# Performance work log

Measured on AMD Instinct MI355X. Metric: run time of the kernel, lower is better.

The kernel has to match this reference:

```python
import jax, jax.numpy as jnp
import numpy as np

HEADS = 8
DIM = 512
DIM_HEAD = 64          # dim // 8
LANDMARKS = 256        # dim // 2
PINV_ITERS = 6
KERNEL = 33            # residual depthwise conv kernel
EPS_LN = 1e-5


def setup_inputs() -> dict:
    key = jax.random.key(0)
    ks = jax.random.split(key, 4)
    b, n = 4, 4096
    x = jax.random.normal(ks[0], (b, n, DIM), dtype=jnp.float32)
    ln_g = jnp.ones((DIM,), jnp.float32)
    ln_b = jnp.zeros((DIM,), jnp.float32)
    w_qkv = jax.random.normal(ks[1], (3 * HEADS * DIM_HEAD, DIM), jnp.float32) * 0.02
    w_out = jax.random.normal(ks[2], (DIM, HEADS * DIM_HEAD), jnp.float32) * 0.02
    b_out = jnp.zeros((DIM,), jnp.float32)
    res_w = jax.random.normal(ks[3], (HEADS, 1, KERNEL, 1), jnp.float32) * 0.05
    return {"x": x, "ln_g": ln_g, "ln_b": ln_b, "w_qkv": w_qkv,
            "w_out": w_out, "b_out": b_out, "res_w": res_w}


def _moore_penrose_pinv(x, iters):
    # x: [b, h, m, m]; global (whole-tensor) max of row/col abs-sums, as in torch impl
    abs_x = jnp.abs(x)
    col = abs_x.sum(-1).max()
    row = abs_x.sum(-2).max()
    z = jnp.swapaxes(x, -1, -2) / (col * row)
    I = jnp.eye(x.shape[-1], dtype=x.dtype)
    for _ in range(iters):
        xz = x @ z
        z = 0.25 * z @ (13.0 * I - (xz @ (15.0 * I - (xz @ (7.0 * I - xz)))))
    return z


def reference(x, ln_g, ln_b, w_qkv, w_out, b_out, res_w):
    b, n, d = x.shape
    # pre-norm LayerNorm
    mu = x.mean(-1, keepdims=True)
    var = ((x - mu) ** 2).mean(-1, keepdims=True)
    xn = (x - mu) * jax.lax.rsqrt(var + EPS_LN) * ln_g + ln_b

    qkv = xn @ w_qkv.T                                  # [b, n, 3*h*dh]
    q, k, v = jnp.split(qkv, 3, axis=-1)
    to_heads = lambda t: t.reshape(b, n, HEADS, DIM_HEAD).transpose(0, 2, 1, 3)
    q = to_heads(q) * (DIM_HEAD ** -0.5)                # [b, h, n, dh]
    k = to_heads(k)
    v = to_heads(v)

    m = LANDMARKS
    l = n // m                                          # n chosen multiple of m (no pad)
    q_l = q.reshape(b, HEADS, m, l, DIM_HEAD).mean(3)   # [b, h, m, dh]
    k_l = k.reshape(b, HEADS, m, l, DIM_HEAD).mean(3)

    attn1 = jax.nn.softmax(jnp.einsum('bhid,bhjd->bhij', q, k_l), -1)    # [b,h,n,m]
    attn2 = jax.nn.softmax(jnp.einsum('bhid,bhjd->bhij', q_l, k_l), -1)  # [b,h,m,m]
    attn3 = jax.nn.softmax(jnp.einsum('bhid,bhjd->bhij', q_l, k), -1)    # [b,h,m,n]

    attn2_inv = _moore_penrose_pinv(attn2, PINV_ITERS)
    out = (attn1 @ attn2_inv) @ (attn3 @ v)             # [b, h, n, dh]

    # residual depthwise conv over sequence dim: v as NCHW (C=heads, H=n, W=dh)
    pad = KERNEL // 2
    res = jax.lax.conv_general_dilated(
        v, res_w, window_strides=(1, 1), padding=((pad, pad), (0, 0)),
        dimension_numbers=('NCHW', 'OIHW', 'NCHW'), feature_group_count=HEADS)
    out = out + res

    out = out.transpose(0, 2, 1, 3).reshape(b, n, HEADS * DIM_HEAD)
    out = out @ w_out.T + b_out                         # to_out Linear (dropout=eval identity)
    return x + out
```

## Files before the change

kernel.cpp:

```cpp
#include <hip/hip_runtime.h>
#include <hip/hip_bf16.h>
#include <math.h>


using bf16x8 = __attribute__((ext_vector_type(8))) short;
using f32x4  = __attribute__((ext_vector_type(4))) float;

static __device__ __forceinline__ f32x4 MFMA16(bf16x8 a, bf16x8 b, f32x4 c) {
    return __builtin_amdgcn_mfma_f32_16x16x32_bf16(a, b, c, 0, 0, 0);
}
static __device__ __forceinline__ unsigned short f2b(float f) {
    union { float f; unsigned u; } x; x.f = f;
    unsigned r = x.u + 0x7FFFu + ((x.u >> 16) & 1u);
    return (unsigned short)(r >> 16);
}
static __device__ __forceinline__ float b2f(unsigned short b) {
    union { unsigned u; float f; } x; x.u = ((unsigned)b) << 16; return x.f;
}

__global__ __launch_bounds__(256) void ln_kernel(const float* __restrict__ x,
                                                 const float* __restrict__ g,
                                                 const float* __restrict__ b,
                                                 unsigned short* __restrict__ xn) {
    int row = blockIdx.x;
    const float* xr = x + (size_t)row * 512;
    int t = threadIdx.x;
    float v0 = xr[t], v1 = xr[t + 256];
    __shared__ float red[4];
    float s = v0 + v1;
#pragma unroll
    for (int off = 32; off; off >>= 1) s += __shfl_down(s, off);
    if ((t & 63) == 0) red[t >> 6] = s;
    __syncthreads();
    float mean = (red[0] + red[1] + red[2] + red[3]) * (1.0f / 512.0f);
    __syncthreads();
    float d0 = v0 - mean, d1 = v1 - mean;
    float q2 = d0 * d0 + d1 * d1;
#pragma unroll
    for (int off = 32; off; off >>= 1) q2 += __shfl_down(q2, off);
    if ((t & 63) == 0) red[t >> 6] = q2;
    __syncthreads();
    float var = (red[0] + red[1] + red[2] + red[3]) * (1.0f / 512.0f);
    float inv = rsqrtf(var + 1e-5f);
    unsigned short* o = xn + (size_t)row * 512;
    o[t]       = f2b(d0 * inv * g[t]       + b[t]);
    o[t + 256] = f2b(d1 * inv * g[t + 256] + b[t + 256]);
}

__global__ void cvt_kernel(const float* __restrict__ wqkv, const float* __restrict__ wout,
                           unsigned short* __restrict__ wqkvb, unsigned short* __restrict__ woutb) {
    int idx = blockIdx.x * 256 + threadIdx.x;
    if (idx < 786432) wqkvb[idx] = f2b(wqkv[idx]);
    else woutb[idx - 786432] = f2b(wout[idx - 786432]);
}

template<int MODE>
__global__ __launch_bounds__(256) void gemm_mfma(const unsigned short* __restrict__ A,
                                                 const unsigned short* __restrict__ Bw,
                                                 unsigned short* __restrict__ qb,
                                                 unsigned short* __restrict__ kb,
                                                 unsigned short* __restrict__ vb,
                                                 const float* __restrict__ bias,
                                                 const float* __restrict__ xres,
                                                 float* __restrict__ out) {
    const int K = 512;
    __shared__ unsigned short As[128][40];
    __shared__ unsigned short Bs[128][40];
    int t = threadIdx.x;
    int w = t >> 6, l = t & 63, lr = l & 15, g = l >> 4;
    int wm = w >> 1, wn = w & 1;
    int row0 = blockIdx.x * 128, col0 = blockIdx.y * 128;
    f32x4 acc[4][4];
#pragma unroll
    for (int i = 0; i < 4; ++i)
#pragma unroll
        for (int j = 0; j < 4; ++j) acc[i][j] = (f32x4)0.f;
    int srow = t >> 1, sh = t & 1;
    for (int kt = 0; kt < K; kt += 32) {
        const unsigned short* as = A + (size_t)(row0 + srow) * K + kt + sh * 16;
        *(uint4*)&As[srow][sh * 16]     = *(const uint4*)as;
        *(uint4*)&As[srow][sh * 16 + 8] = *(const uint4*)(as + 8);
        const unsigned short* bs = Bw + (size_t)(col0 + srow) * K + kt + sh * 16;
        *(uint4*)&Bs[srow][sh * 16]     = *(const uint4*)bs;
        *(uint4*)&Bs[srow][sh * 16 + 8] = *(const uint4*)(bs + 8);
        __syncthreads();
        bf16x8 a[4], b[4];
#pragma unroll
        for (int mt = 0; mt < 4; ++mt) a[mt] = *(const bf16x8*)&As[wm * 64 + mt * 16 + lr][g * 8];
#pragma unroll
        for (int nt = 0; nt < 4; ++nt) b[nt] = *(const bf16x8*)&Bs[wn * 64 + nt * 16 + lr][g * 8];
#pragma unroll
        for (int mt = 0; mt < 4; ++mt)
#pragma unroll
            for (int nt = 0; nt < 4; ++nt) acc[mt][nt] = MFMA16(a[mt], b[nt], acc[mt][nt]);
        __syncthreads();
    }
#pragma unroll
    for (int mt = 0; mt < 4; ++mt) {
#pragma unroll
        for (int nt = 0; nt < 4; ++nt) {
#pragma unroll
            for (int r = 0; r < 4; ++r) {
                int row = row0 + wm * 64 + mt * 16 + g * 4 + r;
                int col = col0 + wn * 64 + nt * 16 + lr;
                float val = acc[mt][nt][r];
                if (MODE == 0) {
                    int bb = row >> 12, nn = row & 4095;
                    int which = col >> 9, rem = col & 511;
                    int hh = rem >> 6, dd = rem & 63;
                    size_t di = (((size_t)(bb * 8 + hh)) * 4096 + nn) * 64 + dd;
                    if (which == 0) qb[di] = f2b(val * 0.125f);
                    else if (which == 1) kb[di] = f2b(val);
                    else vb[di] = f2b(val);
                } else {
                    out[(size_t)row * 512 + col] = val + bias[col] + xres[(size_t)row * 512 + col];
                }
            }
        }
    }
}

__global__ __launch_bounds__(256) void vt_kernel(const unsigned short* __restrict__ vb,
                                                 unsigned short* __restrict__ vtb) {
    int n0 = blockIdx.x * 64, bh = blockIdx.y;
    __shared__ unsigned short tl[64][72];
    int t = threadIdx.x;
#pragma unroll
    for (int u = 0; u < 2; ++u) {
        int cid = t * 2 + u;
        int r = cid >> 3, c8 = (cid & 7) << 3;
        uint4 vv = *(const uint4*)(vb + ((size_t)bh * 4096 + n0 + r) * 64 + c8);
        unsigned short* pv = (unsigned short*)&vv;
#pragma unroll
        for (int i = 0; i < 8; ++i) tl[c8 + i][r] = pv[i];
    }
    __syncthreads();
#pragma unroll
    for (int u = 0; u < 2; ++u) {
        int cid = t * 2 + u;
        int r = cid >> 3, c8 = (cid & 7) << 3;
        *(uint4*)(vtb + ((size_t)bh * 64 + r) * 4096 + n0 + c8) = *(uint4*)&tl[r][c8];
    }
}

__global__ void landmark_kernel(const unsigned short* __restrict__ q,
                                const unsigned short* __restrict__ k,
                                float* __restrict__ ql, float* __restrict__ kl,
                                unsigned short* __restrict__ qlb, unsigned short* __restrict__ klb) {
    int idx = blockIdx.x * 256 + threadIdx.x;
    int dh = idx & 63, mi = (idx >> 6) & 255, bh = idx >> 14;
    size_t base = ((size_t)bh * 4096 + mi * 16) * 64 + dh;
    float sq = 0, sk = 0;
#pragma unroll
    for (int j = 0; j < 16; ++j) { sq += b2f(q[base + (size_t)j * 64]); sk += b2f(k[base + (size_t)j * 64]); }
    sq *= 0.0625f; sk *= 0.0625f;
    ql[idx] = sq; kl[idx] = sk;
    qlb[idx] = f2b(sq); klb[idx] = f2b(sk);
}

__global__ __launch_bounds__(256) void conv_kernel(const unsigned short* __restrict__ v,
                                                   const float* __restrict__ rw,
                                                   float* __restrict__ outh) {
    int idx = blockIdx.x * 256 + threadIdx.x;
    int o = idx & 7, n = (idx >> 3) & 4095, bh = idx >> 15;
    int h = bh & 7;
    const unsigned short* vb = v + (((size_t)bh) << 18) + o * 8;
    float acc[8];
#pragma unroll
    for (int i = 0; i < 8; ++i) acc[i] = 0.f;
#pragma unroll
    for (int tt = 0; tt < 33; ++tt) {
        int j = n + tt - 16;
        if (j >= 0 && j < 4096) {
            uint4 pv = *(const uint4*)(vb + (size_t)j * 64);
            const unsigned short* pp = (const unsigned short*)&pv;
            float wgt = rw[h * 33 + tt];
#pragma unroll
            for (int i = 0; i < 8; ++i) acc[i] = fmaf(wgt, b2f(pp[i]), acc[i]);
        }
    }
    float4 r0, r1;
    r0.x = acc[0]; r0.y = acc[1]; r0.z = acc[2]; r0.w = acc[3];
    r1.x = acc[4]; r1.y = acc[5]; r1.z = acc[6]; r1.w = acc[7];
    *(float4*)(outh + (size_t)idx * 8)     = r0;
    *(float4*)(outh + (size_t)idx * 8 + 4) = r1;
}

__global__ __launch_bounds__(256) void attn2_kernel(const float* __restrict__ ql,
                                                    const float* __restrict__ kl,
                                                    float* __restrict__ a2) {
    int bh = blockIdx.x >> 8, i = blockIdx.x & 255;
    int t = threadIdx.x;
    __shared__ float qrow[64];
    __shared__ float red[4];
    if (t < 64) qrow[t] = ql[((size_t)bh * 256 + i) * 64 + t];
    __syncthreads();
    const float* krow = kl + ((size_t)bh * 256 + t) * 64;
    float s = 0;
#pragma unroll
    for (int c = 0; c < 64; c += 4) {
        float4 kv = *(const float4*)(krow + c);
        s = fmaf(qrow[c], kv.x, s); s = fmaf(qrow[c + 1], kv.y, s);
        s = fmaf(qrow[c + 2], kv.z, s); s = fmaf(qrow[c + 3], kv.w, s);
    }
    float p = __expf(s);
    float sum = p;
#pragma unroll
    for (int off = 32; off; off >>= 1) sum += __shfl_down(sum, off);
    if ((t & 63) == 0) red[t >> 6] = sum;
    __syncthreads();
    float tot = red[0] + red[1] + red[2] + red[3];
    a2[((size_t)bh * 256 + i) * 256 + t] = p / tot;
}

__global__ __launch_bounds__(256) void colmax_kernel(const float* __restrict__ a2,
                                                     unsigned* __restrict__ scal) {
    int bh = blockIdx.x, t = threadIdx.x;
    const float* m = a2 + (size_t)bh * 65536;
    float cs = 0;
    for (int i = 0; i < 256; ++i) cs += m[i * 256 + t];
#pragma unroll
    for (int off = 32; off; off >>= 1) cs = fmaxf(cs, __shfl_down(cs, off));
    __shared__ float red[4];
    if ((t & 63) == 0) red[t >> 6] = cs;
    __syncthreads();
    if (t == 0) {
        float mx = fmaxf(fmaxf(red[0], red[1]), fmaxf(red[2], red[3]));
        atomicMax(scal, __float_as_uint(mx));
    }
}

__global__ __launch_bounds__(256) void z0_kernel(const float* __restrict__ a2,
                                                 const float* __restrict__ scal,
                                                 float* __restrict__ z) {
    int bh = blockIdx.z;
    int ib = blockIdx.x * 64, jb = blockIdx.y * 64;
    __shared__ float tl[64][65];
    float c = 1.0f / *scal;
    int t = threadIdx.x;
#pragma unroll
    for (int u = 0; u < 16; ++u) {
        int idx = t + 256 * u;
        int r = idx >> 6, cc = idx & 63;
        tl[r][cc] = a2[(size_t)bh * 65536 + (size_t)(jb + r) * 256 + ib + cc];
    }
    __syncthreads();
#pragma unroll
    for (int u = 0; u < 16; ++u) {
        int idx = t + 256 * u;
        int r = idx >> 6, cc = idx & 63;
        z[(size_t)bh * 65536 + (size_t)(ib + r) * 256 + jb + cc] = tl[cc][r] * c;
    }
}

__global__ __launch_bounds__(256) void bgemm_mfma_split(const float* __restrict__ A,
                                                        const float* __restrict__ B,
                                                        float* __restrict__ D,
                                                        const float* __restrict__ E,
                                                        float alpha, float gamma) {
    int s = blockIdx.z;
    A += (size_t)s * 65536; B += (size_t)s * 65536; D += (size_t)s * 65536;
    const float* Ep = E ? E + (size_t)s * 65536 : nullptr;
    __shared__ unsigned short Ah[64][40], Al[64][40], Bh[64][40], Bl[64][40];
    int t = threadIdx.x;
    int w = t >> 6, l = t & 63, lr = l & 15, g = l >> 4;
    int wm = w >> 1, wn = w & 1;
    int bm = blockIdx.x, bn = blockIdx.y;
    f32x4 acc[2][2];
#pragma unroll
    for (int i = 0; i < 2; ++i)
#pragma unroll
        for (int j = 0; j < 2; ++j) acc[i][j] = (f32x4)0.f;
    int arow = t >> 2, akq = (t & 3) * 8;
    int bkr = t >> 3, bnq = (t & 7) * 8;
    for (int kt = 0; kt < 256; kt += 32) {
        const float* ap = A + (size_t)(bm * 64 + arow) * 256 + kt + akq;
        float4 a0 = *(const float4*)ap;
        float4 a1 = *(const float4*)(ap + 4);
        float av[8] = {a0.x, a0.y, a0.z, a0.w, a1.x, a1.y, a1.z, a1.w};
#pragma unroll
        for (int i = 0; i < 8; ++i) {
            unsigned short hi = f2b(av[i]);
            Ah[arow][akq + i] = hi;
            Al[arow][akq + i] = f2b(av[i] - b2f(hi));
        }
        const float* bp = B + (size_t)(kt + bkr) * 256 + bn * 64 + bnq;
        float4 b0 = *(const float4*)bp;
        float4 b1 = *(const float4*)(bp + 4);
        float bv[8] = {b0.x, b0.y, b0.z, b0.w, b1.x, b1.y, b1.z, b1.w};
#pragma unroll
        for (int i = 0; i < 8; ++i) {
            unsigned short hi = f2b(bv[i]);
            Bh[bnq + i][bkr] = hi;
            Bl[bnq + i][bkr] = f2b(bv[i] - b2f(hi));
        }
        __syncthreads();
        bf16x8 ah[2], al_[2], bh[2], bl_[2];
#pragma unroll
        for (int mf = 0; mf < 2; ++mf) {
            ah[mf]  = *(const bf16x8*)&Ah[wm * 32 + mf * 16 + lr][g * 8];
            al_[mf] = *(const bf16x8*)&Al[wm * 32 + mf * 16 + lr][g * 8];
        }
#pragma unroll
        for (int nf = 0; nf < 2; ++nf) {
            bh[nf]  = *(const bf16x8*)&Bh[wn * 32 + nf * 16 + lr][g * 8];
            bl_[nf] = *(const bf16x8*)&Bl[wn * 32 + nf * 16 + lr][g * 8];
        }
#pragma unroll
        for (int mf = 0; mf < 2; ++mf)
#pragma unroll
            for (int nf = 0; nf < 2; ++nf) {
                acc[mf][nf] = MFMA16(ah[mf], bh[nf], acc[mf][nf]);
                acc[mf][nf] = MFMA16(ah[mf], bl_[nf], acc[mf][nf]);
                acc[mf][nf] = MFMA16(al_[mf], bh[nf], acc[mf][nf]);
            }
        __syncthreads();
    }
#pragma unroll
    for (int mf = 0; mf < 2; ++mf) {
#pragma unroll
        for (int nf = 0; nf < 2; ++nf) {
#pragma unroll
            for (int r = 0; r < 4; ++r) {
                int row = bm * 64 + wm * 32 + mf * 16 + g * 4 + r;
                int col = bn * 64 + wn * 32 + nf * 16 + lr;
                float val = alpha * acc[mf][nf][r];
                if (Ep) val = fmaf(gamma, Ep[(size_t)row * 256 + col], val);
                D[(size_t)row * 256 + col] = val;
            }
        }
    }
}

__global__ __launch_bounds__(256) void bgemm_w2t(const float* __restrict__ A,
                                                 const float* __restrict__ B,
                                                 unsigned short* __restrict__ w2t) {
    const int M = 256, N = 64, K = 256;
    int s = blockIdx.z;
    int bm = blockIdx.x;
    A += (size_t)s * M * K; B += (size_t)s * K * N;
    __shared__ float As[32][67];
    __shared__ float Bs[32][68];
    int t = threadIdx.x;
    int tm = t & 15, tn = t >> 4;
    float acc[4][4];
#pragma unroll
    for (int i = 0; i < 4; ++i)
#pragma unroll
        for (int j = 0; j < 4; ++j) acc[i][j] = 0.f;
    for (int kt = 0; kt < K; kt += 32) {
#pragma unroll
        for (int u = 0; u < 2; ++u) {
            int fid = t + 256 * u;
            int r = fid >> 3, kg = (fid & 7) << 2;
            float4 av = *(const float4*)(A + (size_t)(bm * 64 + r) * K + kt + kg);
            As[kg + 0][r] = av.x; As[kg + 1][r] = av.y; As[kg + 2][r] = av.z; As[kg + 3][r] = av.w;
            int kr = fid >> 4, cg = (fid & 15) << 2;
            if (cg < N) {
                float4 bv = *(const float4*)(B + (size_t)(kt + kr) * N + cg);
                *(float4*)(&Bs[kr][cg]) = bv;
            }
        }
        __syncthreads();
#pragma unroll
        for (int kk = 0; kk < 32; ++kk) {
            float a[4], bb[4];
#pragma unroll
            for (int i = 0; i < 4; ++i) a[i] = As[kk][tm * 4 + i];
#pragma unroll
            for (int j = 0; j < 4; ++j) bb[j] = Bs[kk][(tn & 15) * 4 + j];
#pragma unroll
            for (int i = 0; i < 4; ++i)
#pragma unroll
                for (int j = 0; j < 4; ++j) acc[i][j] = fmaf(a[i], bb[j], acc[i][j]);
        }
        __syncthreads();
    }
    if (tn < 16) {
#pragma unroll
        for (int i = 0; i < 4; ++i) {
            int r = bm * 64 + tm * 4 + i;
#pragma unroll
            for (int j = 0; j < 4; ++j) {
                int c = tn * 4 + j;
                w2t[(size_t)s * 16384 + (size_t)c * 256 + r] = f2b(acc[i][j]);
            }
        }
    }
}

__global__ __launch_bounds__(256) void attn3v_mfma(const unsigned short* __restrict__ qlb,
                                                   const unsigned short* __restrict__ kb,
                                                   const unsigned short* __restrict__ vtb,
                                                   float* __restrict__ num_part,
                                                   float* __restrict__ den_part) {
    int it = blockIdx.x, js = blockIdx.y, bh = blockIdx.z;
    __shared__ unsigned short k_lds[64][72];
    __shared__ unsigned short v_lds[64][72];
    __shared__ unsigned short p_lds[4][16][72];
    int t = threadIdx.x;
    int w = t >> 6, l = t & 63, lr = l & 15, g = l >> 4;
    int i0 = it * 64;
    const unsigned short* qp = qlb + ((size_t)(bh * 256 + i0 + w * 16 + lr)) * 64 + g * 8;
    bf16x8 aq0 = *(const bf16x8*)qp;
    bf16x8 aq1 = *(const bf16x8*)(qp + 32);
    f32x4 acc[4];
#pragma unroll
    for (int i = 0; i < 4; ++i) acc[i] = (f32x4)0.f;
    float dacc[4] = {0.f, 0.f, 0.f, 0.f};
    int srow = t >> 2, sq = t & 3;
    const size_t kbase = ((size_t)bh * 4096 + js * 1024) * 64;
    const size_t vbase = (size_t)bh * 64 * 4096 + js * 1024;
    for (int st = 0; st < 16; ++st) {
        int j0 = st * 64;
        {
            const unsigned short* src = kb + kbase + (size_t)(j0 + srow) * 64 + sq * 16;
            *(uint4*)&k_lds[srow][sq * 16]     = *(const uint4*)src;
            *(uint4*)&k_lds[srow][sq * 16 + 8] = *(const uint4*)(src + 8);
            const unsigned short* sv = vtb + vbase + (size_t)srow * 4096 + j0 + sq * 16;
            *(uint4*)&v_lds[srow][sq * 16]     = *(const uint4*)sv;
            *(uint4*)&v_lds[srow][sq * 16 + 8] = *(const uint4*)(sv + 8);
        }
        __syncthreads();
        f32x4 sacc[4];
#pragma unroll
        for (int jt = 0; jt < 4; ++jt) {
            bf16x8 bk0 = *(const bf16x8*)&k_lds[jt * 16 + lr][g * 8];
            bf16x8 bk1 = *(const bf16x8*)&k_lds[jt * 16 + lr][32 + g * 8];
            sacc[jt] = MFMA16(aq0, bk0, (f32x4)0.f);
            sacc[jt] = MFMA16(aq1, bk1, sacc[jt]);
        }
        float dr[4] = {0.f, 0.f, 0.f, 0.f};
#pragma unroll
        for (int jt = 0; jt < 4; ++jt) {
#pragma unroll
            for (int r = 0; r < 4; ++r) {
                float p = __expf(sacc[jt][r]);
                p_lds[w][g * 4 + r][jt * 16 + lr] = f2b(p);
                dr[r] += p;
            }
        }
#pragma unroll
        for (int r = 0; r < 4; ++r) {
#pragma unroll
            for (int m = 1; m < 16; m <<= 1) dr[r] += __shfl_xor(dr[r], m);
            dacc[r] += dr[r];
        }
        bf16x8 pa0 = *(const bf16x8*)&p_lds[w][lr][g * 8];
        bf16x8 pa1 = *(const bf16x8*)&p_lds[w][lr][32 + g * 8];
#pragma unroll
        for (int dt = 0; dt < 4; ++dt) {
            bf16x8 bv0 = *(const bf16x8*)&v_lds[dt * 16 + lr][g * 8];
            bf16x8 bv1 = *(const bf16x8*)&v_lds[dt * 16 + lr][32 + g * 8];
            acc[dt] = MFMA16(pa0, bv0, acc[dt]);
            acc[dt] = MFMA16(pa1, bv1, acc[dt]);
        }
        __syncthreads();
    }
    size_t obase = (size_t)(js * 32 + bh) * 256 + i0 + w * 16;
#pragma unroll
    for (int dt = 0; dt < 4; ++dt)
#pragma unroll
        for (int r = 0; r < 4; ++r)
            num_part[(obase + g * 4 + r) * 64 + dt * 16 + lr] = acc[dt][r];
    if (lr == 0) {
#pragma unroll
        for (int r = 0; r < 4; ++r) den_part[obase + g * 4 + r] = dacc[r];
    }
}

__global__ void a3v_combine(const float* __restrict__ num_part,
                            const float* __restrict__ den_part,
                            float* __restrict__ a3v) {
    int idx = blockIdx.x * 256 + threadIdx.x;
    int dh = idx & 63;
    int rest = idx >> 6;
    float n = 0, d = 0;
#pragma unroll
    for (int s = 0; s < 4; ++s) {
        n += num_part[((size_t)s * 8192 + rest) * 64 + dh];
        d += den_part[(size_t)s * 8192 + rest];
    }
    a3v[idx] = n / d;
}

__global__ __launch_bounds__(256) void attn1_mfma(const unsigned short* __restrict__ qb,
                                                  const unsigned short* __restrict__ klb,
                                                  const unsigned short* __restrict__ w2t,
                                                  const float* __restrict__ outh,
                                                  unsigned short* __restrict__ outhb) {
    int it = blockIdx.x, bh = blockIdx.y;
    __shared__ unsigned short k_lds[64][72];
    __shared__ unsigned short v_lds[64][72];
    __shared__ unsigned short p_lds[4][16][72];
    int t = threadIdx.x;
    int w = t >> 6, l = t & 63, lr = l & 15, g = l >> 4;
    int i0 = it * 64;
    const unsigned short* qp = qb + ((size_t)bh * 4096 + i0 + w * 16 + lr) * 64 + g * 8;
    bf16x8 aq0 = *(const bf16x8*)qp;
    bf16x8 aq1 = *(const bf16x8*)(qp + 32);
    f32x4 acc[4];
#pragma unroll
    for (int i = 0; i < 4; ++i) acc[i] = (f32x4)0.f;
    float dacc[4] = {0.f, 0.f, 0.f, 0.f};
    int srow = t >> 2, sq = t & 3;
    for (int st = 0; st < 4; ++st) {
        int j0 = st * 64;
        {
            const unsigned short* src = klb + ((size_t)bh * 256 + j0 + srow) * 64 + sq * 16;
            *(uint4*)&k_lds[srow][sq * 16]     = *(const uint4*)src;
            *(uint4*)&k_lds[srow][sq * 16 + 8] = *(const uint4*)(src + 8);
            const unsigned short* sv = w2t + ((size_t)bh * 64 + srow) * 256 + j0 + sq * 16;
            *(uint4*)&v_lds[srow][sq * 16]     = *(const uint4*)sv;
            *(uint4*)&v_lds[srow][sq * 16 + 8] = *(const uint4*)(sv + 8);
        }
        __syncthreads();
        f32x4 sacc[4];
#pragma unroll
        for (int jt = 0; jt < 4; ++jt) {
            bf16x8 bk0 = *(const bf16x8*)&k_lds[jt * 16 + lr][g * 8];
            bf16x8 bk1 = *(const bf16x8*)&k_lds[jt * 16 + lr][32 + g * 8];
            sacc[jt] = MFMA16(aq0, bk0, (f32x4)0.f);
            sacc[jt] = MFMA16(aq1, bk1, sacc[jt]);
        }
        float dr[4] = {0.f, 0.f, 0.f, 0.f};
#pragma unroll
        for (int jt = 0; jt < 4; ++jt) {
#pragma unroll
            for (int r = 0; r < 4; ++r) {
                float p = __expf(sacc[jt][r]);
                p_lds[w][g * 4 + r][jt * 16 + lr] = f2b(p);
                dr[r] += p;
            }
        }
#pragma unroll
        for (int r = 0; r < 4; ++r) {
#pragma unroll
            for (int m = 1; m < 16; m <<= 1) dr[r] += __shfl_xor(dr[r], m);
            dacc[r] += dr[r];
        }
        bf16x8 pa0 = *(const bf16x8*)&p_lds[w][lr][g * 8];
        bf16x8 pa1 = *(const bf16x8*)&p_lds[w][lr][32 + g * 8];
#pragma unroll
        for (int dt = 0; dt < 4; ++dt) {
            bf16x8 bv0 = *(const bf16x8*)&v_lds[dt * 16 + lr][g * 8];
            bf16x8 bv1 = *(const bf16x8*)&v_lds[dt * 16 + lr][32 + g * 8];
            acc[dt] = MFMA16(pa0, bv0, acc[dt]);
            acc[dt] = MFMA16(pa1, bv1, acc[dt]);
        }
        __syncthreads();
    }
    int bb = bh >> 3, hh = bh & 7;
#pragma unroll
    for (int dt = 0; dt < 4; ++dt) {
#pragma unroll
        for (int r = 0; r < 4; ++r) {
            int row = i0 + w * 16 + g * 4 + r;
            float val = acc[dt][r] / dacc[r]
                      + outh[((size_t)bh * 4096 + row) * 64 + dt * 16 + lr];
            outhb[((size_t)(bb * 4096 + row)) * 512 + hh * 64 + dt * 16 + lr] = f2b(val);
        }
    }
}

extern "C" void kernel_launch(void* const* d_in, const int* in_sizes, int n_in,
                              void* d_out, int out_size, void* d_ws, size_t ws_size,
                              hipStream_t stream) {
    (void)in_sizes; (void)n_in; (void)out_size; (void)ws_size;
    const float* x     = (const float*)d_in[0];
    const float* ln_g  = (const float*)d_in[1];
    const float* ln_b  = (const float*)d_in[2];
    const float* w_qkv = (const float*)d_in[3];
    const float* w_out = (const float*)d_in[4];
    const float* b_out = (const float*)d_in[5];
    const float* res_w = (const float*)d_in[6];
    float* out = (float*)d_out;

    float* ws = (float*)d_ws;
    unsigned short* xnb = (unsigned short*)ws;
    float* outh = ws + 4194304;
    float* ql   = ws + 12582912;
    float* kl   = ws + 13107200;
    float* a2   = ws + 13631488;
    float* z0b  = ws + 15728640;
    float* z1b  = ws + 17825792;
    float* xzb  = ws + 19922944;
    float* t1b  = ws + 22020096;
    float* t2b  = ws + 24117248;
    float* num_part = ws + 26214400;
    float* den_part = ws + 28311552;
    float* a3v  = ws + 28344320;
    unsigned* scal = (unsigned*)(ws + 28868608);
    unsigned short* qb    = (unsigned short*)(ws + 28868612);
    unsigned short* kb    = (unsigned short*)(ws + 33062916);
    unsigned short* vb    = (unsigned short*)(ws + 37257220);
    unsigned short* vtb   = (unsigned short*)(ws + 41451524);
    unsigned short* outhb = (unsigned short*)(ws + 45645828);
    unsigned short* qlb   = (unsigned short*)(ws + 49840132);
    unsigned short* klb   = (unsigned short*)(ws + 50102276);
    unsigned short* wqkvb = (unsigned short*)(ws + 50364420);
    unsigned short* woutb = (unsigned short*)(ws + 50757636);
    unsigned short* w2tb  = (unsigned short*)(ws + 50888708);

    hipMemsetAsync(scal, 0, 4, stream);
    ln_kernel<<<16384, 256, 0, stream>>>(x, ln_g, ln_b, xnb);
    cvt_kernel<<<4096, 256, 0, stream>>>(w_qkv, w_out, wqkvb, woutb);
    gemm_mfma<0><<<dim3(128, 12), 256, 0, stream>>>(xnb, wqkvb, qb, kb, vb, nullptr, nullptr, nullptr);
    vt_kernel<<<dim3(64, 32), 256, 0, stream>>>(vb, vtb);
    landmark_kernel<<<2048, 256, 0, stream>>>(qb, kb, ql, kl, qlb, klb);
    conv_kernel<<<4096, 256, 0, stream>>>(vb, res_w, outh);
    attn2_kernel<<<8192, 256, 0, stream>>>(ql, kl, a2);
    colmax_kernel<<<32, 256, 0, stream>>>(a2, scal);
    z0_kernel<<<dim3(4, 4, 32), 256, 0, stream>>>(a2, (const float*)scal, z0b);
    float* zc = z0b; float* za = z1b;
    for (int itr = 0; itr < 6; ++itr) {
        bgemm_mfma_split<<<dim3(4, 4, 32), 256, 0, stream>>>(a2, zc, xzb, nullptr, 1.f, 0.f);
        bgemm_mfma_split<<<dim3(4, 4, 32), 256, 0, stream>>>(xzb, xzb, t1b, xzb, -1.f, 7.f);
        bgemm_mfma_split<<<dim3(4, 4, 32), 256, 0, stream>>>(xzb, t1b, t2b, xzb, -1.f, 15.f);
        bgemm_mfma_split<<<dim3(4, 4, 32), 256, 0, stream>>>(zc, t2b, za, zc, -0.25f, 3.25f);
        float* tmp = zc; zc = za; za = tmp;
    }
    attn3v_mfma<<<dim3(4, 4, 32), 256, 0, stream>>>(qlb, kb, vtb, num_part, den_part);
    a3v_combine<<<2048, 256, 0, stream>>>(num_part, den_part, a3v);
    bgemm_w2t<<<dim3(4, 1, 32), 256, 0, stream>>>(zc, a3v, w2tb);
    attn1_mfma<<<dim3(64, 32), 256, 0, stream>>>(qb, klb, w2tb, outh, outhb);
    gemm_mfma<1><<<dim3(128, 4), 256, 0, stream>>>(outhb, woutb, nullptr, nullptr, nullptr, b_out, x, out);
}
```

Before: 815.3 us.

## Pre-split pinv operands into bf16 hi/lo pairs and use MFMA for attn2

The Newton-Schulz GEMMs now read pre-split bf16 hi/lo operands written by the previous GEMM's epilogue, instead of loading fp32 and splitting inside every tile load. A split kernel and a split-emitting z0 kernel supply the initial operands. The attn2 landmark scores move from a scalar per-thread dot-product kernel to a split-bf16 MFMA kernel, and the workspace is re-laid out with some buffers aliased. This trades redundant conversion work and fp32 traffic for extra bf16 stores in the epilogues. Intermediate scratch fp32 writes still occur, and the aliasing of a2 as scratch relies on a2 not being needed afterwards.

```diff
diff --git a/kernel.cpp b/kernel.cpp
--- a/kernel.cpp
+++ b/kernel.cpp
@@ -146,7 +146,8 @@
 __global__ void landmark_kernel(const unsigned short* __restrict__ q,
                                 const unsigned short* __restrict__ k,
                                 float* __restrict__ ql, float* __restrict__ kl,
-                                unsigned short* __restrict__ qlb, unsigned short* __restrict__ klb) {
+                                unsigned short* __restrict__ qlb, unsigned short* __restrict__ klb,
+                                unsigned short* __restrict__ qll, unsigned short* __restrict__ kll) {
     int idx = blockIdx.x * 256 + threadIdx.x;
     int dh = idx & 63, mi = (idx >> 6) & 255, bh = idx >> 14;
     size_t base = ((size_t)bh * 4096 + mi * 16) * 64 + dh;
@@ -155,7 +156,10 @@
     for (int j = 0; j < 16; ++j) { sq += b2f(q[base + (size_t)j * 64]); sk += b2f(k[base + (size_t)j * 64]); }
     sq *= 0.0625f; sk *= 0.0625f;
     ql[idx] = sq; kl[idx] = sk;
-    qlb[idx] = f2b(sq); klb[idx] = f2b(sk);
+    unsigned short qh = f2b(sq), kh = f2b(sk);
+    qlb[idx] = qh; klb[idx] = kh;
+    qll[idx] = f2b(sq - b2f(qh));
+    kll[idx] = f2b(sk - b2f(kh));
 }
 
 __global__ __launch_bounds__(256) void conv_kernel(const unsigned short* __restrict__ v,
@@ -186,31 +190,75 @@
     *(float4*)(outh + (size_t)idx * 8 + 4) = r1;
 }
 
-__global__ __launch_bounds__(256) void attn2_kernel(const float* __restrict__ ql,
-                                                    const float* __restrict__ kl,
-                                                    float* __restrict__ a2) {
-    int bh = blockIdx.x >> 8, i = blockIdx.x & 255;
-    int t = threadIdx.x;
-    __shared__ float qrow[64];
-    __shared__ float red[4];
-    if (t < 64) qrow[t] = ql[((size_t)bh * 256 + i) * 64 + t];
-    __syncthreads();
-    const float* krow = kl + ((size_t)bh * 256 + t) * 64;
-    float s = 0;
-#pragma unroll
-    for (int c = 0; c < 64; c += 4) {
-        float4 kv = *(const float4*)(krow + c);
-        s = fmaf(qrow[c], kv.x, s); s = fmaf(qrow[c + 1], kv.y, s);
-        s = fmaf(qrow[c + 2], kv.z, s); s = fmaf(qrow[c + 3], kv.w, s);
-    }
-    float p = __expf(s);
-    float sum = p;
-#pragma unroll
-    for (int off = 32; off; off >>= 1) sum += __shfl_down(sum, off);
-    if ((t & 63) == 0) red[t >> 6] = sum;
-    __syncthreads();
-    float tot = red[0] + red[1] + red[2] + red[3];
-    a2[((size_t)bh * 256 + i) * 256 + t] = p / tot;
+__global__ __launch_bounds__(256) void attn2_mfma(const unsigned short* __restrict__ qlh,
+                                                  const unsigned short* __restrict__ qllo,
+                                                  const unsigned short* __restrict__ klh,
+                                                  const unsigned short* __restrict__ kllo,
+                                                  float* __restrict__ a2) {
+    int it = blockIdx.x, bh = blockIdx.y;
+    __shared__ unsigned short qh_l[64][72], ql_l[64][72];
+    __shared__ unsigned short kh_l[128][72], kl_l[128][72];
+    int t = threadIdx.x;
+    int w = t >> 6, l = t & 63, lr = l & 15, g = l >> 4;
+    int i0 = it * 64;
+    int srow = t >> 2, sq = t & 3;
+    {
+        size_t gi = ((size_t)bh * 256 + i0 + srow) * 64 + sq * 16;
+        *(uint4*)&qh_l[srow][sq * 16]     = *(const uint4*)(qlh + gi);
+        *(uint4*)&qh_l[srow][sq * 16 + 8] = *(const uint4*)(qlh + gi + 8);
+        *(uint4*)&ql_l[srow][sq * 16]     = *(const uint4*)(qllo + gi);
+        *(uint4*)&ql_l[srow][sq * 16 + 8] = *(const uint4*)(qllo + gi + 8);
+    }
+    f32x4 p[16];
+    float tsum[4] = {0.f, 0.f, 0.f, 0.f};
+    bf16x8 ah0, ah1, al0, al1;
+#pragma unroll
+    for (int ph = 0; ph < 2; ++ph) {
+        __syncthreads();
+#pragma unroll
+        for (int st = 0; st < 2; ++st) {
+            int row = st * 64 + srow;
+            size_t gi = ((size_t)bh * 256 + ph * 128 + row) * 64 + sq * 16;
+            *(uint4*)&kh_l[row][sq * 16]     = *(const uint4*)(klh + gi);
+            *(uint4*)&kh_l[row][sq * 16 + 8] = *(const uint4*)(klh + gi + 8);
+            *(uint4*)&kl_l[row][sq * 16]     = *(const uint4*)(kllo + gi);
+            *(uint4*)&kl_l[row][sq * 16 + 8] = *(const uint4*)(kllo + gi + 8);
+        }
+        __syncthreads();
+        if (ph == 0) {
+            ah0 = *(const bf16x8*)&qh_l[w * 16 + lr][g * 8];
+            ah1 = *(const bf16x8*)&qh_l[w * 16 + lr][32 + g * 8];
+            al0 = *(const bf16x8*)&ql_l[w * 16 + lr][g * 8];
+            al1 = *(const bf16x8*)&ql_l[w * 16 + lr][32 + g * 8];
+        }
+#pragma unroll
+        for (int f = 0; f < 8; ++f) {
+            bf16x8 bh0 = *(const bf16x8*)&kh_l[f * 16 + lr][g * 8];
+            bf16x8 bh1 = *(const bf16x8*)&kh_l[f * 16 + lr][32 + g * 8];
+            bf16x8 bl0 = *(const bf16x8*)&kl_l[f * 16 + lr][g * 8];
+            bf16x8 bl1 = *(const bf16x8*)&kl_l[f * 16 + lr][32 + g * 8];
+            f32x4 s = (f32x4)0.f;
+            s = MFMA16(ah0, bh0, s); s = MFMA16(ah1, bh1, s);
+            s = MFMA16(ah0, bl0, s); s = MFMA16(ah1, bl1, s);
+            s = MFMA16(al0, bh0, s); s = MFMA16(al1, bh1, s);
+            f32x4 pe;
+#pragma unroll
+            for (int r = 0; r < 4; ++r) { pe[r] = __expf(s[r]); tsum[r] += pe[r]; }
+            p[ph * 8 + f] = pe;
+        }
+    }
+#pragma unroll
+    for (int r = 0; r < 4; ++r) {
+#pragma unroll
+        for (int m = 1; m < 16; m <<= 1) tsum[r] += __shfl_xor(tsum[r], m);
+    }
+#pragma unroll
+    for (int f = 0; f < 16; ++f) {
+#pragma unroll
+        for (int r = 0; r < 4; ++r) {
+            a2[((size_t)bh * 256 + i0 + w * 16 + g * 4 + r) * 256 + f * 16 + lr] = p[f][r] / tsum[r];
+        }
+    }
 }
 
 __global__ __launch_bounds__(256) void colmax_kernel(const float* __restrict__ a2,
@@ -230,9 +278,11 @@
     }
 }
 
-__global__ __launch_bounds__(256) void z0_kernel(const float* __restrict__ a2,
-                                                 const float* __restrict__ scal,
-                                                 float* __restrict__ z) {
+__global__ __launch_bounds__(256) void z0_split(const float* __restrict__ a2,
+                                                const float* __restrict__ scal,
+                                                float* __restrict__ zf,
+                                                unsigned short* __restrict__ zh,
+                                                unsigned short* __restrict__ zl) {
     int bh = blockIdx.z;
     int ib = blockIdx.x * 64, jb = blockIdx.y * 64;
     __shared__ float tl[64][65];
@@ -249,19 +299,47 @@
     for (int u = 0; u < 16; ++u) {
         int idx = t + 256 * u;
         int r = idx >> 6, cc = idx & 63;
-        z[(size_t)bh * 65536 + (size_t)(ib + r) * 256 + jb + cc] = tl[cc][r] * c;
-    }
-}
-
-__global__ __launch_bounds__(256) void bgemm_mfma_split(const float* __restrict__ A,
-                                                        const float* __restrict__ B,
-                                                        float* __restrict__ D,
-                                                        const float* __restrict__ E,
-                                                        float alpha, float gamma) {
-    int s = blockIdx.z;
-    A += (size_t)s * 65536; B += (size_t)s * 65536; D += (size_t)s * 65536;
-    const float* Ep = E ? E + (size_t)s * 65536 : nullptr;
-    __shared__ unsigned short Ah[64][40], Al[64][40], Bh[64][40], Bl[64][40];
+        float v = tl[cc][r] * c;
+        unsigned short hi = f2b(v);
+        size_t di = (size_t)bh * 65536 + (size_t)(ib + r) * 256 + jb + cc;
+        zf[di] = v;
+        zh[di] = hi;
+        zl[di] = f2b(v - b2f(hi));
+    }
+}
+
+__global__ void split_kernel(const float* __restrict__ src,
+                             unsigned short* __restrict__ dh,
+                             unsigned short* __restrict__ dl) {
+    int idx4 = (blockIdx.x * 256 + threadIdx.x) * 4;
+    float4 v = *(const float4*)(src + idx4);
+    float vv[4] = {v.x, v.y, v.z, v.w};
+    ushort4 h4, l4;
+    unsigned short* hp = (unsigned short*)&h4;
+    unsigned short* lp = (unsigned short*)&l4;
+#pragma unroll
+    for (int j = 0; j < 4; ++j) {
+        unsigned short hi = f2b(vv[j]);
+        hp[j] = hi;
+        lp[j] = f2b(vv[j] - b2f(hi));
+    }
+    *(ushort4*)(dh + idx4) = h4;
+    *(ushort4*)(dl + idx4) = l4;
+}
+
+__global__ __launch_bounds__(256) void bgemm_split2(const unsigned short* __restrict__ Ahg,
+                                                    const unsigned short* __restrict__ Alg,
+                                                    const unsigned short* __restrict__ Bhg,
+                                                    const unsigned short* __restrict__ Blg,
+                                                    unsigned short* __restrict__ Dh,
+                                                    unsigned short* __restrict__ Dl,
+                                                    float* __restrict__ Df,
+                                                    const float* __restrict__ Ef,
+                                                    float alpha, float gamma) {
+    size_t so = (size_t)blockIdx.z * 65536;
+    Ahg += so; Alg += so; Bhg += so; Blg += so; Dh += so; Dl += so; Df += so;
+    const float* Efp = Ef ? Ef + so : nullptr;
+    __shared__ unsigned short Ah[64][40], Al[64][40], Bh2[64][40], Bl2[64][40];
     int t = threadIdx.x;
     int w = t >> 6, l = t & 63, lr = l & 15, g = l >> 4;
     int wm = w >> 1, wn = w & 1;
@@ -274,25 +352,18 @@
     int arow = t >> 2, akq = (t & 3) * 8;
     int bkr = t >> 3, bnq = (t & 7) * 8;
     for (int kt = 0; kt < 256; kt += 32) {
-        const float* ap = A + (size_t)(bm * 64 + arow) * 256 + kt + akq;
-        float4 a0 = *(const float4*)ap;
-        float4 a1 = *(const float4*)(ap + 4);
-        float av[8] = {a0.x, a0.y, a0.z, a0.w, a1.x, a1.y, a1.z, a1.w};
+        size_t ai = (size_t)(bm * 64 + arow) * 256 + kt + akq;
+        *(uint4*)&Ah[arow][akq] = *(const uint4*)(Ahg + ai);
+        *(uint4*)&Al[arow][akq] = *(const uint4*)(Alg + ai);
+        size_t bi = (size_t)(kt + bkr) * 256 + bn * 64 + bnq;
+        uint4 bhv = *(const uint4*)(Bhg + bi);
+        uint4 blv = *(const uint4*)(Blg + bi);
+        const unsigned short* bhp = (const unsigned short*)&bhv;
+        const unsigned short* blp = (const unsigned short*)&blv;
 #pragma unroll
         for (int i = 0; i < 8; ++i) {
-            unsigned short hi = f2b(av[i]);
-            Ah[arow][akq + i] = hi;
-            Al[arow][akq + i] = f2b(av[i] - b2f(hi));
-        }
-        const float* bp = B + (size_t)(kt + bkr) * 256 + bn * 64 + bnq;
-        float4 b0 = *(const float4*)bp;
-        float4 b1 = *(const float4*)(bp + 4);
-        float bv[8] = {b0.x, b0.y, b0.z, b0.w, b1.x, b1.y, b1.z, b1.w};
-#pragma unroll
-        for (int i = 0; i < 8; ++i) {
-            unsigned short hi = f2b(bv[i]);
-            Bh[bnq + i][bkr] = hi;
-            Bl[bnq + i][bkr] = f2b(bv[i] - b2f(hi));
+            Bh2[bnq + i][bkr] = bhp[i];
+            Bl2[bnq + i][bkr] = blp[i];
         }
         __syncthreads();
         bf16x8 ah[2], al_[2], bh[2], bl_[2];
@@ -303,8 +374,8 @@
         }
 #pragma unroll
         for (int nf = 0; nf < 2; ++nf) {
-            bh[nf]  = *(const bf16x8*)&Bh[wn * 32 + nf * 16 + lr][g * 8];
-            bl_[nf] = *(const bf16x8*)&Bl[wn * 32 + nf * 16 + lr][g * 8];
+            bh[nf]  = *(const bf16x8*)&Bh2[wn * 32 + nf * 16 + lr][g * 8];
+            bl_[nf] = *(const bf16x8*)&Bl2[wn * 32 + nf * 16 + lr][g * 8];
         }
 #pragma unroll
         for (int mf = 0; mf < 2; ++mf)
@@ -324,9 +395,13 @@
             for (int r = 0; r < 4; ++r) {
                 int row = bm * 64 + wm * 32 + mf * 16 + g * 4 + r;
                 int col = bn * 64 + wn * 32 + nf * 16 + lr;
+                size_t di = (size_t)row * 256 + col;
                 float val = alpha * acc[mf][nf][r];
-                if (Ep) val = fmaf(gamma, Ep[(size_t)row * 256 + col], val);
-                D[(size_t)row * 256 + col] = val;
+                if (Efp) val = fmaf(gamma, Efp[di], val);
+                Df[di] = val;
+                unsigned short hi = f2b(val);
+                Dh[di] = hi;
+                Dl[di] = f2b(val - b2f(hi));
             }
         }
     }
@@ -578,51 +653,68 @@
 
     float* ws = (float*)d_ws;
     unsigned short* xnb = (unsigned short*)ws;
+    float* num_part = ws;
+    float* den_part = ws + 2097152;
+    float* a3v      = ws + 2129920;
+    unsigned short* outhb = (unsigned short*)ws;
     float* outh = ws + 4194304;
     float* ql   = ws + 12582912;
     float* kl   = ws + 13107200;
     float* a2   = ws + 13631488;
-    float* z0b  = ws + 15728640;
-    float* z1b  = ws + 17825792;
-    float* xzb  = ws + 19922944;
-    float* t1b  = ws + 22020096;
-    float* t2b  = ws + 24117248;
-    float* num_part = ws + 26214400;
-    float* den_part = ws + 28311552;
-    float* a3v  = ws + 28344320;
-    unsigned* scal = (unsigned*)(ws + 28868608);
-    unsigned short* qb    = (unsigned short*)(ws + 28868612);
-    unsigned short* kb    = (unsigned short*)(ws + 33062916);
-    unsigned short* vb    = (unsigned short*)(ws + 37257220);
-    unsigned short* vtb   = (unsigned short*)(ws + 41451524);
-    unsigned short* outhb = (unsigned short*)(ws + 45645828);
-    unsigned short* qlb   = (unsigned short*)(ws + 49840132);
-    unsigned short* klb   = (unsigned short*)(ws + 50102276);
-    unsigned short* wqkvb = (unsigned short*)(ws + 50364420);
-    unsigned short* woutb = (unsigned short*)(ws + 50757636);
-    unsigned short* w2tb  = (unsigned short*)(ws + 50888708);
+    float* z0f  = ws + 15728640;
+    float* z1f  = ws + 17825792;
+    float* xzf  = ws + 19922944;
+    unsigned* scal = (unsigned*)(ws + 22020096);
+    unsigned short* a2h = (unsigned short*)(ws + 22020100);
+    unsigned short* a2l = (unsigned short*)(ws + 23068676);
+    unsigned short* z0h = (unsigned short*)(ws + 24117252);
+    unsigned short* z0l = (unsigned short*)(ws + 25165828);
+    unsigned short* z1h = (unsigned short*)(ws + 26214404);
+    unsigned short* z1l = (unsigned short*)(ws + 27262980);
+    unsigned short* xzh = (unsigned short*)(ws + 28311556);
+    unsigned short* xzl = (unsigned short*)(ws + 29360132);
+    unsigned short* t1h = (unsigned short*)(ws + 30408708);
+    unsigned short* t1l = (unsigned short*)(ws + 31457284);
+    unsigned short* t2h = (unsigned short*)(ws + 32505860);
+    unsigned short* t2l = (unsigned short*)(ws + 33554436);
+    unsigned short* qb  = (unsigned short*)(ws + 34603012);
+    unsigned short* kb  = (unsigned short*)(ws + 38797316);
+    unsigned short* vb  = (unsigned short*)(ws + 42991620);
+    unsigned short* vtb = (unsigned short*)(ws + 47185924);
+    unsigned short* qlb   = (unsigned short*)(ws + 51380228);
+    unsigned short* klb   = (unsigned short*)(ws + 51642372);
+    unsigned short* qll   = (unsigned short*)(ws + 51904516);
+    unsigned short* kll   = (unsigned short*)(ws + 52166660);
+    unsigned short* wqkvb = (unsigned short*)(ws + 52428804);
+    unsigned short* woutb = (unsigned short*)(ws + 52822020);
+    unsigned short* w2tb  = (unsigned short*)(ws + 52953092);
 
     hipMemsetAsync(scal, 0, 4, stream);
     ln_kernel<<<16384, 256, 0, stream>>>(x, ln_g, ln_b, xnb);
     cvt_kernel<<<4096, 256, 0, stream>>>(w_qkv, w_out, wqkvb, woutb);
     gemm_mfma<0><<<dim3(128, 12), 256, 0, stream>>>(xnb, wqkvb, qb, kb, vb, nullptr, nullptr, nullptr);
     vt_kernel<<<dim3(64, 32), 256, 0, stream>>>(vb, vtb);
-    landmark_kernel<<<2048, 256, 0, stream>>>(qb, kb, ql, kl, qlb, klb);
+    landmark_kernel<<<2048, 256, 0, stream>>>(qb, kb, ql, kl, qlb, klb, qll, kll);
     conv_kernel<<<4096, 256, 0, stream>>>(vb, res_w, outh);
-    attn2_kernel<<<8192, 256, 0, stream>>>(ql, kl, a2);
+    attn2_mfma<<<dim3(4, 32), 256, 0, stream>>>(qlb, qll, klb, kll, a2);
     colmax_kernel<<<32, 256, 0, stream>>>(a2, scal);
-    z0_kernel<<<dim3(4, 4, 32), 256, 0, stream>>>(a2, (const float*)scal, z0b);
-    float* zc = z0b; float* za = z1b;
+    z0_split<<<dim3(4, 4, 32), 256, 0, stream>>>(a2, (const float*)scal, z0f, z0h, z0l);
+    split_kernel<<<2048, 256, 0, stream>>>(a2, a2h, a2l);
+    unsigned short *zch = z0h, *zcl = z0l, *zah = z1h, *zal = z1l;
+    float *zcf = z0f, *zaf = z1f;
+    float* dfscratch = a2;
     for (int itr = 0; itr < 6; ++itr) {
-        bgemm_mfma_split<<<dim3(4, 4, 32), 256, 0, stream>>>(a2, zc, xzb, nullptr, 1.f, 0.f);
-        bgemm_mfma_split<<<dim3(4, 4, 32), 256, 0, stream>>>(xzb, xzb, t1b, xzb, -1.f, 7.f);
-        bgemm_mfma_split<<<dim3(4, 4, 32), 256, 0, stream>>>(xzb, t1b, t2b, xzb, -1.f, 15.f);
-        bgemm_mfma_split<<<dim3(4, 4, 32), 256, 0, stream>>>(zc, t2b, za, zc, -0.25f, 3.25f);
-        float* tmp = zc; zc = za; za = tmp;
+        bgemm_split2<<<dim3(4, 4, 32), 256, 0, stream>>>(a2h, a2l, zch, zcl, xzh, xzl, xzf, nullptr, 1.f, 0.f);
+        bgemm_split2<<<dim3(4, 4, 32), 256, 0, stream>>>(xzh, xzl, xzh, xzl, t1h, t1l, dfscratch, xzf, -1.f, 7.f);
+        bgemm_split2<<<dim3(4, 4, 32), 256, 0, stream>>>(xzh, xzl, t1h, t1l, t2h, t2l, dfscratch, xzf, -1.f, 15.f);
+        bgemm_split2<<<dim3(4, 4, 32), 256, 0, stream>>>(zch, zcl, t2h, t2l, zah, zal, zaf, zcf, -0.25f, 3.25f);
+        unsigned short* th = zch; zch = zah; zah = th;
+        unsigned short* tl2 = zcl; zcl = zal; zal = tl2;
+        float* tf = zcf; zcf = zaf; zaf = tf;
     }
     attn3v_mfma<<<dim3(4, 4, 32), 256, 0, stream>>>(qlb, kb, vtb, num_part, den_part);
     a3v_combine<<<2048, 256, 0, stream>>>(num_part, den_part, a3v);
-    bgemm_w2t<<<dim3(4, 1, 32), 256, 0, stream>>>(zc, a3v, w2tb);
+    bgemm_w2t<<<dim3(4, 1, 32), 256, 0, stream>>>(zcf, a3v, w2tb);
     attn1_mfma<<<dim3(64, 32), 256, 0, stream>>>(qb, klb, w2tb, outh, outhb);
     gemm_mfma<1><<<dim3(128, 4), 256, 0, stream>>>(outhb, woutb, nullptr, nullptr, nullptr, b_out, x, out);
 }
```

Result: slower. 868.5 us (+6.5%).
